# Performance work log

Measured on AMD Instinct MI355X. Metric: run time of the kernel, lower is better.

Reference implementation:

```python
import jax, jax.numpy as jnp
import numpy as np

SCALING = 1.0


def setup_inputs() -> dict:
    key = jax.random.key(0)
    k1, k2, k3, k4, k5, k6 = jax.random.split(key, 6)
    in_f, out_f, r = 4096, 4096, 32
    nnz = r * (in_f + out_f)  # 262144
    x = jax.random.normal(k1, (4, 2048, in_f), dtype=jnp.float32)
    weight = jax.random.normal(k2, (out_f, in_f), dtype=jnp.float32) * 0.02
    bias = jax.random.normal(k3, (out_f,), dtype=jnp.float32) * 0.02
    shira_weight = jax.random.normal(k4, (nnz,), dtype=jnp.float32) * 0.02
    rows = jax.random.randint(k5, (1, nnz), 0, out_f, dtype=jnp.int32)
    cols = jax.random.randint(k6, (1, nnz), 0, in_f, dtype=jnp.int32)
    shira_indices = jnp.concatenate([rows, cols], axis=0)  # [2, nnz]
    return {"x": x, "weight": weight, "bias": bias,
            "shira_weight": shira_weight, "shira_indices": shira_indices}


def reference(x, weight, bias, shira_weight, shira_indices):
    # delta = sparse_coo(indices, shira_weight * scaling) densified into weight copy
    new_weight = weight.at[shira_indices[0], shira_indices[1]].add(shira_weight * SCALING)
    # F.linear: x @ W^T + b
    return jnp.einsum('bsi,oi->bso', x, new_weight) + bias
```

## Files before the change

### kernel.cpp

```cpp
#include <hip/hip_runtime.h>
#include <hip/hip_bf16.h>
#include <stdint.h>

typedef float v4f __attribute__((ext_vector_type(4)));
typedef short v8s __attribute__((ext_vector_type(8)));

#define GEMM_M 8192
#define GEMM_N 4096
#define GEMM_K 4096
#define BM 128
#define BN 128
#define BK 32


__device__ __forceinline__ uint16_t f2bf(float f) {
    union { float f; uint32_t u; } v; v.f = f;
    uint32_t r = v.u + 0x7FFFu + ((v.u >> 16) & 1u);
    return (uint16_t)(r >> 16);
}

__device__ __forceinline__ float bf2f(uint16_t h) {
    union { uint32_t u; float f; } v; v.u = ((uint32_t)h) << 16;
    return v.f;
}

__device__ __forceinline__ void cvt8(const float* __restrict__ s, uint16_t* __restrict__ d) {
    float4 a = ((const float4*)s)[0];
    float4 b = ((const float4*)s)[1];
    union { v8s v; uint16_t u[8]; } o;
    o.u[0] = f2bf(a.x); o.u[1] = f2bf(a.y); o.u[2] = f2bf(a.z); o.u[3] = f2bf(a.w);
    o.u[4] = f2bf(b.x); o.u[5] = f2bf(b.y); o.u[6] = f2bf(b.z); o.u[7] = f2bf(b.w);
    *(v8s*)d = o.v;
}

__global__ void prep_cvt_kernel(const float* __restrict__ X, const float* __restrict__ W,
                                uint16_t* __restrict__ Xb, uint16_t* __restrict__ Wb,
                                size_t x8) {
    size_t i = (size_t)blockIdx.x * blockDim.x + threadIdx.x;
    if (i < x8) {
        cvt8(X + i * 8, Xb + i * 8);
    } else {
        size_t j = i - x8;
        cvt8(W + j * 8, Wb + j * 8);
    }
}

__global__ void scatter_bf16_kernel(uint16_t* __restrict__ Wb, const float* __restrict__ vals,
                                    const int* __restrict__ rows, const int* __restrict__ cols,
                                    int nnz) {
    int i = blockIdx.x * blockDim.x + threadIdx.x;
    if (i >= nnz) return;
    size_t idx = (size_t)rows[i] * GEMM_K + cols[i];
    uint32_t* addr = (uint32_t*)Wb + (idx >> 1);
    const bool hi = idx & 1;
    const float v = vals[i];
    uint32_t cur = *addr, assumed;
    do {
        assumed = cur;
        uint16_t h = hi ? (uint16_t)(assumed >> 16) : (uint16_t)(assumed & 0xFFFFu);
        uint16_t nh = f2bf(bf2f(h) + v);
        uint32_t nw = hi ? ((assumed & 0x0000FFFFu) | ((uint32_t)nh << 16))
                         : ((assumed & 0xFFFF0000u) | (uint32_t)nh);
        if (nw == assumed) break;
        cur = atomicCAS(addr, assumed, nw);
    } while (cur != assumed);
}


__device__ __forceinline__ void gload_lds16(const void* g, void* lds) {
    __builtin_amdgcn_global_load_lds(
        (const __attribute__((address_space(1))) void*)(uintptr_t)g,
        (__attribute__((address_space(3))) void*)(uintptr_t)lds,
        16, 0, 0);
}

__global__ __launch_bounds__(256) void gemm_bt_kernel(
    const uint16_t* __restrict__ A,
    const uint16_t* __restrict__ B,
    const float* __restrict__ bias,
    float* __restrict__ C)
{
    __shared__ __attribute__((aligned(16))) uint16_t As[BM * BK];
    __shared__ __attribute__((aligned(16))) uint16_t Bs[BN * BK];

    const int tid  = threadIdx.x;
    const int lane = tid & 63;
    const int wv   = tid >> 6;
    const int wy   = wv >> 1;
    const int wx   = wv & 1;
    const int lrow = lane & 15;
    const int quad = lane >> 4;

    const int m0 = blockIdx.y * BM;
    const int n0 = blockIdx.x * BN;

    const int e0 = (wv * 2 + 0) * 64 + lane;
    const int e1 = (wv * 2 + 1) * 64 + lane;
    const uint16_t* a_g0 = A + (size_t)(m0 + (e0 >> 2)) * GEMM_K + (e0 & 3) * 8;
    const uint16_t* a_g1 = A + (size_t)(m0 + (e1 >> 2)) * GEMM_K + (e1 & 3) * 8;
    const uint16_t* b_g0 = B + (size_t)(n0 + (e0 >> 2)) * GEMM_K + (e0 & 3) * 8;
    const uint16_t* b_g1 = B + (size_t)(n0 + (e1 >> 2)) * GEMM_K + (e1 & 3) * 8;
    uint16_t* a_l0 = As + e0 * 8;
    uint16_t* a_l1 = As + e1 * 8;
    uint16_t* b_l0 = Bs + e0 * 8;
    uint16_t* b_l1 = Bs + e1 * 8;

    v4f acc[4][4];
#pragma unroll
    for (int i = 0; i < 4; i++)
#pragma unroll
        for (int j = 0; j < 4; j++) acc[i][j] = (v4f){0.f, 0.f, 0.f, 0.f};

    for (int k0 = 0; k0 < GEMM_K; k0 += BK) {
        gload_lds16(a_g0 + k0, a_l0);
        gload_lds16(a_g1 + k0, a_l1);
        gload_lds16(b_g0 + k0, b_l0);
        gload_lds16(b_g1 + k0, b_l1);
        __syncthreads();

        v8s af[4], bf[4];
#pragma unroll
        for (int t = 0; t < 4; t++)
            af[t] = *(const v8s*)(As + (wy * 64 + t * 16 + lrow) * BK + quad * 8);
#pragma unroll
        for (int t = 0; t < 4; t++)
            bf[t] = *(const v8s*)(Bs + (wx * 64 + t * 16 + lrow) * BK + quad * 8);

#pragma unroll
        for (int i = 0; i < 4; i++)
#pragma unroll
            for (int j = 0; j < 4; j++)
                acc[i][j] = __builtin_amdgcn_mfma_f32_16x16x32_bf16(af[i], bf[j], acc[i][j], 0, 0, 0);

        __syncthreads();
    }

#pragma unroll
    for (int j = 0; j < 4; j++) {
        const int col = n0 + wx * 64 + j * 16 + lrow;
        const float bj = bias[col];
#pragma unroll
        for (int i = 0; i < 4; i++) {
            const int row = m0 + wy * 64 + i * 16 + quad * 4;
            float* cp = C + (size_t)row * GEMM_N + col;
#pragma unroll
            for (int r = 0; r < 4; r++)
                cp[(size_t)r * GEMM_N] = acc[i][j][r] + bj;
        }
    }
}


extern "C" void kernel_launch(void* const* d_in, const int* in_sizes, int n_in,
                              void* d_out, int out_size, void* d_ws, size_t ws_size,
                              hipStream_t stream) {
    const float* x      = (const float*)d_in[0];
    const float* weight = (const float*)d_in[1];
    const float* bias   = (const float*)d_in[2];
    const float* sw     = (const float*)d_in[3];
    const int*   sidx   = (const int*)d_in[4];
    const int nnz = in_sizes[3];

    const size_t welems = (size_t)GEMM_N * GEMM_K;
    const size_t xelems = (size_t)GEMM_M * GEMM_K;

    uint16_t* Wb = (uint16_t*)d_ws;
    uint16_t* Xb = (uint16_t*)((char*)d_ws + welems * sizeof(uint16_t));

    const size_t x8 = xelems / 8;
    const size_t w8 = welems / 8;
    const int prep_blocks = (int)((x8 + w8) / 256);

    prep_cvt_kernel<<<dim3(prep_blocks), 256, 0, stream>>>(x, weight, Xb, Wb, x8);
    scatter_bf16_kernel<<<dim3((nnz + 255) / 256), 256, 0, stream>>>(
        Wb, sw, sidx, sidx + nnz, nnz);
    gemm_bt_kernel<<<dim3(GEMM_N / BN, GEMM_M / BM), 256, 0, stream>>>(
        Xb, Wb, bias, (float*)d_out);
}
```

Baseline: 596.6 us.

## Double K tile to 64 and XOR-swizzle LDS layout for bf16 GEMM

Raises BK from 32 to 64 so each barrier pair covers twice the MFMA work, which halves the main-loop iteration and synchronisation count. Global-to-LDS loads are redistributed so each thread issues 4 loads per operand. The 16-byte chunk index within each row is XOR-swizzled by row so that fragment reads avoid LDS bank conflicts. LDS use doubles, which may reduce occupancy.

After: 593.9 us. No clear change (-0.5%).

```diff
diff --git a/kernel.cpp b/kernel.cpp
--- a/kernel.cpp
+++ b/kernel.cpp
@@ -10,7 +10,7 @@
 #define GEMM_K 4096
 #define BM 128
 #define BN 128
-#define BK 32
+#define BK 64
 
 
 __device__ __forceinline__ uint16_t f2bf(float f) {
@@ -94,16 +94,12 @@
     const int m0 = blockIdx.y * BM;
     const int n0 = blockIdx.x * BN;
 
-    const int e0 = (wv * 2 + 0) * 64 + lane;
-    const int e1 = (wv * 2 + 1) * 64 + lane;
-    const uint16_t* a_g0 = A + (size_t)(m0 + (e0 >> 2)) * GEMM_K + (e0 & 3) * 8;
-    const uint16_t* a_g1 = A + (size_t)(m0 + (e1 >> 2)) * GEMM_K + (e1 & 3) * 8;
-    const uint16_t* b_g0 = B + (size_t)(n0 + (e0 >> 2)) * GEMM_K + (e0 & 3) * 8;
-    const uint16_t* b_g1 = B + (size_t)(n0 + (e1 >> 2)) * GEMM_K + (e1 & 3) * 8;
-    uint16_t* a_l0 = As + e0 * 8;
-    uint16_t* a_l1 = As + e1 * 8;
-    uint16_t* b_l0 = Bs + e0 * 8;
-    uint16_t* b_l1 = Bs + e1 * 8;
+    const int srow = wv * 32 + (lane >> 3);
+    const int skc  = ((lane & 7) ^ (lane >> 3)) * 8;
+    const uint16_t* a_g = A + (size_t)(m0 + srow) * GEMM_K + skc;
+    const uint16_t* b_g = B + (size_t)(n0 + srow) * GEMM_K + skc;
+    uint16_t* a_l = As + (size_t)(wv * 256 + lane) * 8;
+    uint16_t* b_l = Bs + (size_t)(wv * 256 + lane) * 8;
 
     v4f acc[4][4];
 #pragma unroll
@@ -111,26 +107,35 @@
 #pragma unroll
         for (int j = 0; j < 4; j++) acc[i][j] = (v4f){0.f, 0.f, 0.f, 0.f};
 
+    const int xr = lrow & 7;
+
     for (int k0 = 0; k0 < GEMM_K; k0 += BK) {
-        gload_lds16(a_g0 + k0, a_l0);
-        gload_lds16(a_g1 + k0, a_l1);
-        gload_lds16(b_g0 + k0, b_l0);
-        gload_lds16(b_g1 + k0, b_l1);
+#pragma unroll
+        for (int i = 0; i < 4; i++) {
+            gload_lds16(a_g + k0 + (size_t)i * 8 * GEMM_K, a_l + i * 512);
+            gload_lds16(b_g + k0 + (size_t)i * 8 * GEMM_K, b_l + i * 512);
+        }
         __syncthreads();
 
-        v8s af[4], bf[4];
 #pragma unroll
-        for (int t = 0; t < 4; t++)
-            af[t] = *(const v8s*)(As + (wy * 64 + t * 16 + lrow) * BK + quad * 8);
+        for (int h = 0; h < 2; h++) {
+            v8s af[4], bf[4];
 #pragma unroll
-        for (int t = 0; t < 4; t++)
-            bf[t] = *(const v8s*)(Bs + (wx * 64 + t * 16 + lrow) * BK + quad * 8);
-
+            for (int t = 0; t < 4; t++) {
+                const int row = wy * 64 + t * 16 + lrow;
+                af[t] = *(const v8s*)(As + row * BK + (((h * 4 + quad) ^ xr) * 8));
+            }
 #pragma unroll
-        for (int i = 0; i < 4; i++)
+            for (int t = 0; t < 4; t++) {
+                const int row = wx * 64 + t * 16 + lrow;
+                bf[t] = *(const v8s*)(Bs + row * BK + (((h * 4 + quad) ^ xr) * 8));
+            }
 #pragma unroll
-            for (int j = 0; j < 4; j++)
-                acc[i][j] = __builtin_amdgcn_mfma_f32_16x16x32_bf16(af[i], bf[j], acc[i][j], 0, 0, 0);
+            for (int i = 0; i < 4; i++)
+#pragma unroll
+                for (int j = 0; j < 4; j++)
+                    acc[i][j] = __builtin_amdgcn_mfma_f32_16x16x32_bf16(af[i], bf[j], acc[i][j], 0, 0, 0);
+        }
 
         __syncthreads();
     }
```
